# Performance work log

Hardware: AMD Instinct MI355X
Metric: run time of the kernel (lower is better)

The kernel has to match this reference:

```python
import jax, jax.numpy as jnp
import numpy as np

D_MODEL = 1024
D_HID = 4096
NUM_EXPERTS = 8
TOP_K = 2


def setup_inputs() -> dict:
    key = jax.random.key(0)
    ks = jax.random.split(key, 6)
    B, T = 4, 1024
    x = jax.random.normal(ks[0], (B, T, D_MODEL), dtype=jnp.float32)
    # router gate: nn.Linear(d_model, num_experts, bias=False) -> weight [E, D]
    gate_w = jax.random.normal(ks[1], (NUM_EXPERTS, D_MODEL), dtype=jnp.float32) / np.sqrt(D_MODEL)
    # expert FFN weights (kaiming-uniform-ish scale)
    lim1 = np.sqrt(6.0 / D_MODEL)
    lim2 = np.sqrt(6.0 / D_HID)
    w1 = jax.random.uniform(ks[2], (NUM_EXPERTS, D_MODEL, D_HID), jnp.float32, -lim1, lim1)
    b1 = jnp.zeros((NUM_EXPERTS, 1, D_HID), jnp.float32)
    w2 = jax.random.uniform(ks[3], (NUM_EXPERTS, D_HID, D_MODEL), jnp.float32, -lim2, lim2)
    b2 = jnp.zeros((NUM_EXPERTS, 1, D_MODEL), jnp.float32)
    return {"x": x, "gate_w": gate_w, "w1": w1, "b1": b1, "w2": w2, "b2": b2}


def reference(x, gate_w, w1, b1, w2, b2):
    B, T, D = x.shape
    E = w1.shape[0]
    xf = x.reshape(-1, D)                       # [N, D]
    N = xf.shape[0]

    # ---- TopKRouter ----
    router_logits = xf @ gate_w.T               # [N, E]
    scores = jax.nn.softmax(router_logits, axis=-1)
    top_w, top_i = jax.lax.top_k(scores, TOP_K)  # [N, K]
    top_w = top_w / jnp.sum(top_w, axis=-1, keepdims=True)

    # ---- expert FFN (dense all-experts compute + sparse gated combine) ----
    # h: [E, N, H]; b1 [E,1,H] broadcasts over tokens
    h = jax.nn.gelu(jnp.einsum('nd,edh->enh', xf, w1) + b1, approximate=False)
    y = jnp.einsum('enh,ehd->end', h, w2) + b2   # [E, N, D]

    # sparse gate matrix: [N, E], nonzero only at top-k experts per token
    gate = jnp.zeros((N, E), dtype=xf.dtype).at[jnp.arange(N)[:, None], top_i].set(top_w)
    out = jnp.einsum('end,ne->nd', y, gate)      # weighted combine
    return out.reshape(B, T, D)
```

## Files before the change

kernel.cpp:

```cpp
#include <hip/hip_runtime.h>
#include <hip/hip_bf16.h>
#include <math.h>

#define D_MODEL 1024
#define D_HID   4096
#define NE      8
#define NTOK    4096
#define NSLOT   8192

typedef __attribute__((ext_vector_type(8))) short s8v;
typedef __attribute__((ext_vector_type(4))) float f32x4;

__device__ __forceinline__ short f2bf(float f) {
    unsigned u = __float_as_uint(f);
    unsigned r = (u + 0x7fffu + ((u >> 16) & 1u)) >> 16;
    return (short)r;
}

__device__ __forceinline__ float bf2f(short s) {
    unsigned u = ((unsigned)(unsigned short)s) << 16;
    return __uint_as_float(u);
}

__device__ __forceinline__ void load_lds16(const short* g, short* l) {
    __builtin_amdgcn_global_load_lds(
        (const __attribute__((address_space(1))) void*)g,
        (__attribute__((address_space(3))) void*)l, 16, 0, 0);
}

__device__ __forceinline__ float gelu_t(float v) {
    float u = v * fmaf(0.0356774081f, v * v, 0.7978845608f);
    float e = __expf(-2.0f * u);
    return v * __builtin_amdgcn_rcpf(1.0f + e);
}


__global__ __launch_bounds__(256) void k_cvt_router(
    const float* __restrict__ x, const float* __restrict__ gw,
    short* __restrict__ xb,
    int* __restrict__ tki, float* __restrict__ tkw) {
    int n = blockIdx.x * 4 + (threadIdx.x >> 6);
    int lane = threadIdx.x & 63;
    const float4* x4 = (const float4*)x;
    const float4* g4 = (const float4*)gw;
    float4 xv[4];
    #pragma unroll
    for (int j = 0; j < 4; j++) xv[j] = x4[(size_t)n * 256 + lane + 64 * j];
    #pragma unroll
    for (int j = 0; j < 4; j++) {
        short4 o;
        o.x = f2bf(xv[j].x); o.y = f2bf(xv[j].y);
        o.z = f2bf(xv[j].z); o.w = f2bf(xv[j].w);
        *(short4*)(xb + (size_t)n * D_MODEL + 4 * (lane + 64 * j)) = o;
    }
    float l[8];
    #pragma unroll
    for (int e = 0; e < 8; e++) {
        float a = 0.f;
        #pragma unroll
        for (int j = 0; j < 4; j++) {
            float4 g = g4[e * 256 + lane + 64 * j];
            a = fmaf(xv[j].x, g.x, a);
            a = fmaf(xv[j].y, g.y, a);
            a = fmaf(xv[j].z, g.z, a);
            a = fmaf(xv[j].w, g.w, a);
        }
        #pragma unroll
        for (int s = 32; s > 0; s >>= 1) a += __shfl_xor(a, s);
        l[e] = a;
    }
    if (lane == 0) {
        float bv = -1e30f, sv = -1e30f; int bi = 0, si = 0;
        #pragma unroll
        for (int e = 0; e < 8; e++) {
            float v = l[e];
            if (v > bv) { sv = bv; si = bi; bv = v; bi = e; }
            else if (v > sv) { sv = v; si = e; }
        }
        float w0 = 1.f / (1.f + expf(sv - bv));
        tki[n * 2] = bi; tki[n * 2 + 1] = si;
        tkw[n * 2] = w0; tkw[n * 2 + 1] = 1.f - w0;
    }
}


__global__ void k_transpose_cvt2(const float* __restrict__ w1, const float* __restrict__ w2,
                                 short* __restrict__ w1t, short* __restrict__ w2t) {
    __shared__ float tile[64][65];
    int z = blockIdx.z;
    int R, C;
    const float* inp;
    short* outp;
    int tIdx = blockIdx.y * 64 + blockIdx.x;
    if (z < 8) {
        R = D_MODEL; C = D_HID;
        inp  = w1  + (size_t)z * R * C;
        outp = w1t + (size_t)z * R * C;
    } else {
        R = D_HID; C = D_MODEL;
        inp  = w2  + (size_t)(z - 8) * R * C;
        outp = w2t + (size_t)(z - 8) * R * C;
    }
    int tilesC = C >> 6;
    int c0 = (tIdx % tilesC) * 64;
    int r0 = (tIdx / tilesC) * 64;
    int t = threadIdx.x;
    #pragma unroll
    for (int p = 0; p < 4; p++) {
        int idx = p * 256 + t;
        int r = idx >> 4;
        int c4 = (idx & 15) * 4;
        float4 v = *(const float4*)(inp + (size_t)(r0 + r) * C + c0 + c4);
        tile[r][c4 + 0] = v.x; tile[r][c4 + 1] = v.y;
        tile[r][c4 + 2] = v.z; tile[r][c4 + 3] = v.w;
    }
    __syncthreads();
    #pragma unroll
    for (int p = 0; p < 4; p++) {
        int idx = p * 256 + t;
        int cc = idx >> 4;
        int rg = (idx & 15) * 4;
        short4 v;
        v.x = f2bf(tile[rg + 0][cc]);
        v.y = f2bf(tile[rg + 1][cc]);
        v.z = f2bf(tile[rg + 2][cc]);
        v.w = f2bf(tile[rg + 3][cc]);
        *(short4*)(outp + (size_t)(c0 + cc) * R + r0 + rg) = v;
    }
}


__global__ __launch_bounds__(1024) void k_bucket(
    const int* __restrict__ tki, const float* __restrict__ tkw,
    int* __restrict__ offs,
    int* __restrict__ list, float* __restrict__ wl, int* __restrict__ slot_of) {
    __shared__ int cnt[NE], base[NE + 1], fil[NE];
    int t = threadIdx.x;
    if (t < NE) { cnt[t] = 0; fil[t] = 0; }
    __syncthreads();
    for (int n = t; n < NTOK; n += 1024) {
        atomicAdd(&cnt[tki[n * 2]], 1);
        atomicAdd(&cnt[tki[n * 2 + 1]], 1);
    }
    __syncthreads();
    if (t == 0) {
        int a = 0;
        for (int e = 0; e < NE; e++) { base[e] = a; a += cnt[e]; }
        base[NE] = a;
    }
    __syncthreads();
    if (t < NE + 1) offs[t] = base[t];
    for (int n = t; n < NTOK; n += 1024) {
        #pragma unroll
        for (int k = 0; k < 2; k++) {
            int e = tki[n * 2 + k];
            int p = base[e] + atomicAdd(&fil[e], 1);
            list[p] = n;
            wl[p] = tkw[n * 2 + k];
            slot_of[n * 2 + k] = p;
        }
    }
}


#define PIPE_WAIT(NSTR) \
    asm volatile("s_waitcnt vmcnt(" NSTR ")" ::: "memory"); \
    __builtin_amdgcn_s_barrier(); \
    __builtin_amdgcn_sched_barrier(0);

#define PIPE_POST \
    asm volatile("" ::: "memory"); \
    __builtin_amdgcn_s_barrier();

#define GEMM_PIPE_LOOP(KDIM, STAGE, COMPUTE, NSTR) \
    STAGE(As0, Bs0); \
    for (int k0 = 0; k0 < (KDIM) - 128; k0 += 128) { \
        STAGE(As1, Bs1); PIPE_WAIT(NSTR) COMPUTE(As0, Bs0) PIPE_POST \
        STAGE(As0, Bs0); PIPE_WAIT(NSTR) COMPUTE(As1, Bs1) PIPE_POST \
    } \
    STAGE(As1, Bs1); PIPE_WAIT(NSTR) COMPUTE(As0, Bs0) PIPE_POST \
    PIPE_WAIT("0") COMPUTE(As1, Bs1)


#define STAGE_T(ABASE, BBASE) \
    { _Pragma("unroll") \
      for (int c = 0; c < 2; c++) { load_lds16(aS[c], (ABASE) + ldsDa[c]); aS[c] += 64; } \
      _Pragma("unroll") \
      for (int c = 0; c < 4; c++) { load_lds16(bS[c], (BBASE) + ldsDb[c]); bS[c] += 64; } }

#define COMPUTE_T(ABASE, BBASE) \
    { _Pragma("unroll") \
      for (int kk = 0; kk < 2; kk++) { \
          s8v a[2], b[4]; \
          _Pragma("unroll") \
          for (int i = 0; i < 2; i++) a[i] = *(const s8v*)((ABASE) + aO[i][kk]); \
          _Pragma("unroll") \
          for (int j = 0; j < 4; j++) b[j] = *(const s8v*)((BBASE) + bO[j][kk]); \
          _Pragma("unroll") \
          for (int i = 0; i < 2; i++) \
              _Pragma("unroll") \
              for (int j = 0; j < 4; j++) \
                  acc[i][j] = __builtin_amdgcn_mfma_f32_16x16x32_bf16(a[i], b[j], acc[i][j], 0, 0, 0); \
      } }

#define FRAG_SETUP_T \
    int tid = threadIdx.x; \
    int lane = tid & 63; \
    int wid = tid >> 6; \
    int wm = wid >> 1, wn = wid & 1; \
    f32x4 acc[2][4] = {}; \
    int aO[2][2], bO[4][2]; \
    _Pragma("unroll") \
    for (int k = 0; k < 2; k++) { \
        int l = k * 4 + (lane >> 4); \
        _Pragma("unroll") \
        for (int i = 0; i < 2; i++) { \
            int R = wm * 32 + i * 16 + (lane & 15); \
            aO[i][k] = R * 64 + ((l ^ (R & 7)) * 8); \
        } \
        _Pragma("unroll") \
        for (int j = 0; j < 4; j++) { \
            int R = wn * 64 + j * 16 + (lane & 15); \
            bO[j][k] = R * 64 + ((l ^ (R & 7)) * 8); \
        } \
    }


__global__ __launch_bounds__(256) void k_gemm1(
    const short* __restrict__ xb,
    const short* __restrict__ w1t,
    const float* __restrict__ b1,
    const int* __restrict__ offs,
    const int* __restrict__ list,
    short* __restrict__ hbuf)
{
    int id = blockIdx.x;
    int w = (id & 7) * 2048 + (id >> 3);
    int e = w >> 11;
    int o0 = offs[e];
    int nE = offs[e + 1] - o0;
    int local = w & 2047;
    int intra = local & 63;
    int chunk = local >> 6;
    int n0 = ((chunk & 3) * 8 + (intra & 7)) * 128;
    int m0 = ((chunk >> 2) * 8 + (intra >> 3)) * 64;
    if (m0 >= nE) return;

    __shared__ short As[64 * 64];
    __shared__ short Bs[128 * 64];

    int tid = threadIdx.x;
    int lane = tid & 63;
    int wid = tid >> 6;
    int wm = wid >> 1, wn = wid & 1;

    f32x4 acc[2][4] = {};

    const short* aS[2]; const short* bS[4];
    int ldsDa[2], ldsDb[4];
    #pragma unroll
    for (int c = 0; c < 2; c++) {
        int i = c * 256 + tid;
        int rowT = i >> 3, s = i & 7;
        int ch = s ^ (rowT & 7);
        int r = m0 + rowT; if (r > nE - 1) r = nE - 1;
        int tok = list[o0 + r];
        aS[c] = xb + (size_t)tok * D_MODEL + ch * 8;
        ldsDa[c] = i * 8;
    }
    #pragma unroll
    for (int c = 0; c < 4; c++) {
        int i = c * 256 + tid;
        int rowT = i >> 3, s = i & 7;
        int ch = s ^ (rowT & 7);
        bS[c] = w1t + ((size_t)e * D_HID + n0 + rowT) * D_MODEL + ch * 8;
        ldsDb[c] = i * 8;
    }

    int aO[2][2], bO[4][2];
    #pragma unroll
    for (int k = 0; k < 2; k++) {
        int l = k * 4 + (lane >> 4);
        #pragma unroll
        for (int i = 0; i < 2; i++) {
            int R = wm * 32 + i * 16 + (lane & 15);
            aO[i][k] = R * 64 + ((l ^ (R & 7)) * 8);
        }
        #pragma unroll
        for (int j = 0; j < 4; j++) {
            int R = wn * 64 + j * 16 + (lane & 15);
            bO[j][k] = R * 64 + ((l ^ (R & 7)) * 8);
        }
    }

    for (int k0 = 0; k0 < D_MODEL; k0 += 64) {
        __syncthreads();
        #pragma unroll
        for (int c = 0; c < 2; c++) { load_lds16(aS[c], As + ldsDa[c]); aS[c] += 64; }
        #pragma unroll
        for (int c = 0; c < 4; c++) { load_lds16(bS[c], Bs + ldsDb[c]); bS[c] += 64; }
        asm volatile("s_waitcnt vmcnt(0)" ::: "memory");
        __syncthreads();
        #pragma unroll
        for (int kk = 0; kk < 2; kk++) {
            s8v a[2], b[4];
            #pragma unroll
            for (int i = 0; i < 2; i++) a[i] = *(const s8v*)(As + aO[i][kk]);
            #pragma unroll
            for (int j = 0; j < 4; j++) b[j] = *(const s8v*)(Bs + bO[j][kk]);
            #pragma unroll
            for (int i = 0; i < 2; i++)
                #pragma unroll
                for (int j = 0; j < 4; j++)
                    acc[i][j] = __builtin_amdgcn_mfma_f32_16x16x32_bf16(a[i], b[j], acc[i][j], 0, 0, 0);
        }
    }

    int rBase = m0 + wm * 32 + (lane >> 4) * 4;
    int cBase = n0 + wn * 64 + (lane & 15);
    #pragma unroll
    for (int i = 0; i < 2; i++) {
        #pragma unroll
        for (int j = 0; j < 4; j++) {
            int cc = cBase + j * 16;
            float bias = b1[e * D_HID + cc];
            #pragma unroll
            for (int rg = 0; rg < 4; rg++) {
                int rr = rBase + i * 16 + rg;
                if (rr < nE) {
                    float v = acc[i][j][rg] + bias;
                    hbuf[(size_t)(o0 + rr) * D_HID + cc] = f2bf(gelu_t(v));
                }
            }
        }
    }
}


__global__ __launch_bounds__(256) void k_gemm2(
    const short* __restrict__ hbuf,
    const short* __restrict__ w2t,
    const float* __restrict__ b2,
    const int* __restrict__ offs,
    const float* __restrict__ wl,
    short* __restrict__ ybuf)
{
    int id = blockIdx.x;
    int w = (id & 7) * 512 + (id >> 3);
    int e = w >> 9;
    int o0 = offs[e];
    int nE = offs[e + 1] - o0;
    int m0 = ((w >> 3) & 63) * 64;
    if (m0 >= nE) return;
    int n0 = (w & 7) * 128;

    __shared__ short As0[64 * 64], Bs0[128 * 64];
    __shared__ short As1[64 * 64], Bs1[128 * 64];

    FRAG_SETUP_T

    const short* aS[2]; const short* bS[4];
    int ldsDa[2], ldsDb[4];
    #pragma unroll
    for (int c = 0; c < 2; c++) {
        int i = c * 256 + tid;
        int rowT = i >> 3, s = i & 7;
        int ch = s ^ (rowT & 7);
        int r = m0 + rowT; if (r > nE - 1) r = nE - 1;
        aS[c] = hbuf + (size_t)(o0 + r) * D_HID + ch * 8;
        ldsDa[c] = i * 8;
    }
    #pragma unroll
    for (int c = 0; c < 4; c++) {
        int i = c * 256 + tid;
        int rowT = i >> 3, s = i & 7;
        int ch = s ^ (rowT & 7);
        bS[c] = w2t + ((size_t)e * D_MODEL + n0 + rowT) * D_HID + ch * 8;
        ldsDb[c] = i * 8;
    }

    GEMM_PIPE_LOOP(D_HID, STAGE_T, COMPUTE_T, "6")

    int rBase = m0 + wm * 32 + (lane >> 4) * 4;
    int cBase = n0 + wn * 64 + (lane & 15);
    #pragma unroll
    for (int i = 0; i < 2; i++) {
        #pragma unroll
        for (int j = 0; j < 4; j++) {
            int cc = cBase + j * 16;
            float bias = b2[e * D_MODEL + cc];
            #pragma unroll
            for (int rg = 0; rg < 4; rg++) {
                int rr = rBase + i * 16 + rg;
                if (rr < nE) {
                    int slot = o0 + rr;
                    float wgt = wl[slot];
                    ybuf[(size_t)slot * D_MODEL + cc] = f2bf(wgt * (acc[i][j][rg] + bias));
                }
            }
        }
    }
}


__global__ void k_combine(const short* __restrict__ ybuf, const int* __restrict__ slot_of,
                          float* __restrict__ out) {
    int n = blockIdx.x;
    int s0 = slot_of[n * 2], s1 = slot_of[n * 2 + 1];
    int t = threadIdx.x;
    short4 a = *(const short4*)(ybuf + (size_t)s0 * D_MODEL + t * 4);
    short4 b = *(const short4*)(ybuf + (size_t)s1 * D_MODEL + t * 4);
    float4 o;
    o.x = bf2f(a.x) + bf2f(b.x);
    o.y = bf2f(a.y) + bf2f(b.y);
    o.z = bf2f(a.z) + bf2f(b.z);
    o.w = bf2f(a.w) + bf2f(b.w);
    *(float4*)(out + (size_t)n * D_MODEL + t * 4) = o;
}


extern "C" void kernel_launch(void* const* d_in, const int* in_sizes, int n_in,
                              void* d_out, int out_size, void* d_ws, size_t ws_size,
                              hipStream_t stream) {
    const float* x  = (const float*)d_in[0];
    const float* gw = (const float*)d_in[1];
    const float* w1 = (const float*)d_in[2];
    const float* b1 = (const float*)d_in[3];
    const float* w2 = (const float*)d_in[4];
    const float* b2 = (const float*)d_in[5];
    float* out = (float*)d_out;

    char* ws = (char*)d_ws;
    size_t off = 0;
    auto alloc = [&](size_t bytes) -> void* {
        void* p = ws + off;
        off += (bytes + 255) & ~(size_t)255;
        return p;
    };
    int*   offs    = (int*)alloc(64);
    int*   tki     = (int*)alloc((size_t)NTOK * 2 * 4);
    float* tkw     = (float*)alloc((size_t)NTOK * 2 * 4);
    int*   list    = (int*)alloc((size_t)NSLOT * 4);
    float* wl      = (float*)alloc((size_t)NSLOT * 4);
    int*   slot_of = (int*)alloc((size_t)NTOK * 2 * 4);
    short* xb      = (short*)alloc((size_t)NTOK * D_MODEL * 2);
    short* w1t     = (short*)alloc((size_t)NE * D_HID * D_MODEL * 2);
    short* w2t     = (short*)alloc((size_t)NE * D_MODEL * D_HID * 2);
    short* hbuf    = (short*)alloc((size_t)NSLOT * D_HID * 2);
    short* ybuf    = (short*)alloc((size_t)NSLOT * D_MODEL * 2);

    k_cvt_router<<<dim3(NTOK / 4), 256, 0, stream>>>(x, gw, xb, tki, tkw);
    k_transpose_cvt2<<<dim3(64, 16, 16), 256, 0, stream>>>(w1, w2, w1t, w2t);
    k_bucket<<<dim3(1), 1024, 0, stream>>>(tki, tkw, offs, list, wl, slot_of);
    k_gemm1<<<dim3(16384), 256, 0, stream>>>(xb, w1t, b1, offs, list, hbuf);
    k_gemm2<<<dim3(4096), 256, 0, stream>>>(hbuf, w2t, b2, offs, wl, ybuf);
    k_combine<<<dim3(NTOK), 256, 0, stream>>>(ybuf, slot_of, out);
}
```

Measured before the change: 318.9 us.

## Pad expert segments to 64 rows and launch compact gemm1 grid

Each expert's slot segment is rounded up to a multiple of 64 and the padding entries are zeroed, so the GEMMs can drop row clamping and bounds checks. gemm1 now walks a global row-tile index over all padded slots and finds the expert by searching offs, which shrinks its grid from 16384 mostly-idle blocks to 4352. The aim is to cut the cost of launching and early-exiting empty blocks and to simplify the epilogues. In exchange it computes up to 63 padding rows per expert and adds a clearing pass over list/wl inside the single-block bucket kernel.

Measured after the change: 299.7 us. 6.0% less time.

```diff
diff --git a/kernel.cpp b/kernel.cpp
--- a/kernel.cpp
+++ b/kernel.cpp
@@ -7,6 +7,7 @@
 #define NE      8
 #define NTOK    4096
 #define NSLOT   8192
+#define NSLOTP  (NSLOT + 512)
 
 typedef __attribute__((ext_vector_type(8))) short s8v;
 typedef __attribute__((ext_vector_type(4))) float f32x4;
@@ -145,11 +146,13 @@
     __syncthreads();
     if (t == 0) {
         int a = 0;
-        for (int e = 0; e < NE; e++) { base[e] = a; a += cnt[e]; }
+        for (int e = 0; e < NE; e++) { base[e] = a; a += (cnt[e] + 63) & ~63; }
         base[NE] = a;
     }
     __syncthreads();
     if (t < NE + 1) offs[t] = base[t];
+    for (int p = t; p < NSLOTP; p += 1024) { list[p] = 0; wl[p] = 0.f; }
+    __syncthreads();
     for (int n = t; n < NTOK; n += 1024) {
         #pragma unroll
         for (int k = 0; k < 2; k++) {
@@ -235,16 +238,20 @@
     short* __restrict__ hbuf)
 {
     int id = blockIdx.x;
-    int w = (id & 7) * 2048 + (id >> 3);
-    int e = w >> 11;
+    int w = (id & 7) * 544 + (id >> 3);
+    int chunk = w >> 6;
+    int intra = w & 63;
+    int nb = (chunk & 3) * 8 + (intra & 7);
+    int mb = (chunk >> 2) * 8 + (intra >> 3);
+    int base = mb * 64;
+    int total = offs[NE];
+    if (base >= total) return;
+    int e = 0;
+    #pragma unroll
+    for (int q = 1; q < NE; q++) e += (base >= offs[q]) ? 1 : 0;
     int o0 = offs[e];
-    int nE = offs[e + 1] - o0;
-    int local = w & 2047;
-    int intra = local & 63;
-    int chunk = local >> 6;
-    int n0 = ((chunk & 3) * 8 + (intra & 7)) * 128;
-    int m0 = ((chunk >> 2) * 8 + (intra >> 3)) * 64;
-    if (m0 >= nE) return;
+    int m0 = base - o0;
+    int n0 = nb * 128;
 
     __shared__ short As[64 * 64];
     __shared__ short Bs[128 * 64];
@@ -263,8 +270,7 @@
         int i = c * 256 + tid;
         int rowT = i >> 3, s = i & 7;
         int ch = s ^ (rowT & 7);
-        int r = m0 + rowT; if (r > nE - 1) r = nE - 1;
-        int tok = list[o0 + r];
+        int tok = list[base + rowT];
         aS[c] = xb + (size_t)tok * D_MODEL + ch * 8;
         ldsDa[c] = i * 8;
     }
@@ -316,7 +322,7 @@
         }
     }
 
-    int rBase = m0 + wm * 32 + (lane >> 4) * 4;
+    int rBase = base + wm * 32 + (lane >> 4) * 4;
     int cBase = n0 + wn * 64 + (lane & 15);
     #pragma unroll
     for (int i = 0; i < 2; i++) {
@@ -327,10 +333,8 @@
             #pragma unroll
             for (int rg = 0; rg < 4; rg++) {
                 int rr = rBase + i * 16 + rg;
-                if (rr < nE) {
-                    float v = acc[i][j][rg] + bias;
-                    hbuf[(size_t)(o0 + rr) * D_HID + cc] = f2bf(gelu_t(v));
-                }
+                float v = acc[i][j][rg] + bias;
+                hbuf[(size_t)rr * D_HID + cc] = f2bf(gelu_t(v));
             }
         }
     }
@@ -366,8 +370,7 @@
         int i = c * 256 + tid;
         int rowT = i >> 3, s = i & 7;
         int ch = s ^ (rowT & 7);
-        int r = m0 + rowT; if (r > nE - 1) r = nE - 1;
-        aS[c] = hbuf + (size_t)(o0 + r) * D_HID + ch * 8;
+        aS[c] = hbuf + (size_t)(o0 + m0 + rowT) * D_HID + ch * 8;
         ldsDa[c] = i * 8;
     }
     #pragma unroll
@@ -392,11 +395,9 @@
             #pragma unroll
             for (int rg = 0; rg < 4; rg++) {
                 int rr = rBase + i * 16 + rg;
-                if (rr < nE) {
-                    int slot = o0 + rr;
-                    float wgt = wl[slot];
-                    ybuf[(size_t)slot * D_MODEL + cc] = f2bf(wgt * (acc[i][j][rg] + bias));
-                }
+                int slot = o0 + rr;
+                float wgt = wl[slot];
+                ybuf[(size_t)slot * D_MODEL + cc] = f2bf(wgt * (acc[i][j][rg] + bias));
             }
         }
     }
@@ -440,19 +441,19 @@
     int*   offs    = (int*)alloc(64);
     int*   tki     = (int*)alloc((size_t)NTOK * 2 * 4);
     float* tkw     = (float*)alloc((size_t)NTOK * 2 * 4);
-    int*   list    = (int*)alloc((size_t)NSLOT * 4);
-    float* wl      = (float*)alloc((size_t)NSLOT * 4);
+    int*   list    = (int*)alloc((size_t)NSLOTP * 4);
+    float* wl      = (float*)alloc((size_t)NSLOTP * 4);
     int*   slot_of = (int*)alloc((size_t)NTOK * 2 * 4);
     short* xb      = (short*)alloc((size_t)NTOK * D_MODEL * 2);
     short* w1t     = (short*)alloc((size_t)NE * D_HID * D_MODEL * 2);
     short* w2t     = (short*)alloc((size_t)NE * D_MODEL * D_HID * 2);
-    short* hbuf    = (short*)alloc((size_t)NSLOT * D_HID * 2);
-    short* ybuf    = (short*)alloc((size_t)NSLOT * D_MODEL * 2);
+    short* hbuf    = (short*)alloc((size_t)NSLOTP * D_HID * 2);
+    short* ybuf    = (short*)alloc((size_t)NSLOTP * D_MODEL * 2);
 
     k_cvt_router<<<dim3(NTOK / 4), 256, 0, stream>>>(x, gw, xb, tki, tkw);
     k_transpose_cvt2<<<dim3(64, 16, 16), 256, 0, stream>>>(w1, w2, w1t, w2t);
     k_bucket<<<dim3(1), 1024, 0, stream>>>(tki, tkw, offs, list, wl, slot_of);
-    k_gemm1<<<dim3(16384), 256, 0, stream>>>(xb, w1t, b1, offs, list, hbuf);
+    k_gemm1<<<dim3(4352), 256, 0, stream>>>(xb, w1t, b1, offs, list, hbuf);
     k_gemm2<<<dim3(4096), 256, 0, stream>>>(hbuf, w2t, b2, offs, wl, ybuf);
     k_combine<<<dim3(NTOK), 256, 0, stream>>>(ybuf, slot_of, out);
 }
```
